# Performance work log

Measured on AMD Instinct MI355X. Metric: run time of the kernel, lower is better.

## Reference

```python
import jax, jax.numpy as jnp
import numpy as np
from jax import lax

NB = 8        # num_branch
K1 = 64       # == K2
NPOINT = 1024 # FPS samples
EPS = 1e-5    # BatchNorm eps


def setup_inputs() -> dict:
    key = jax.random.key(0)
    ks = jax.random.split(key, 40)
    B, L, F = 32, 512, 256
    Npart = 32768
    s = 0.05
    p = lambda k, sh: jax.random.normal(k, sh, jnp.float32) * s
    g = lambda k, sh: 1.0 + jax.random.normal(k, sh, jnp.float32) * 0.05
    inp = {}
    inp['x'] = jax.random.normal(ks[0], (B, L, F), jnp.float32)
    inp['x_part'] = jax.random.normal(ks[1], (B, Npart, 3), jnp.float32)
    # MappingNet params (stacked over NB branches)
    inp['mW1'] = p(ks[2], (NB, 512, 256)); inp['mb1'] = p(ks[3], (NB, 512))
    inp['mg1'] = g(ks[4], (NB, 512));      inp['mB1'] = p(ks[5], (NB, 512))
    inp['mW2'] = p(ks[6], (NB, 512, 512)); inp['mb2'] = p(ks[7], (NB, 512))
    inp['mg2'] = g(ks[8], (NB, 512));      inp['mB2'] = p(ks[9], (NB, 512))
    inp['mW3'] = p(ks[10], (NB, 512, 512)); inp['mb3'] = p(ks[11], (NB, 512))
    inp['mg3'] = g(ks[12], (NB, 512));      inp['mB3'] = p(ks[13], (NB, 512))
    inp['mW4'] = p(ks[14], (NB, K1, 512));  inp['mb4'] = p(ks[15], (NB, K1))
    inp['mg4'] = g(ks[16], (NB, K1));       inp['mB4'] = p(ks[17], (NB, K1))
    # AXform params (1x1 Conv1d == channel matmul), stacked over NB branches
    inp['aW1'] = p(ks[18], (NB, 64, K1));   inp['ab1'] = p(ks[19], (NB, 64))
    inp['ag1'] = g(ks[20], (NB, 64));       inp['aB1'] = p(ks[21], (NB, 64))
    inp['aW2'] = p(ks[22], (NB, 128, 64));  inp['ab2'] = p(ks[23], (NB, 128))
    inp['ag2'] = g(ks[24], (NB, 128));      inp['aB2'] = p(ks[25], (NB, 128))
    inp['aW3'] = p(ks[26], (NB, 128, 128)); inp['ab3'] = p(ks[27], (NB, 128))
    inp['aW4'] = p(ks[28], (NB, 3, K1));    inp['ab4'] = p(ks[29], (NB, 3))
    return inp


def _bn_feat(h, gam, bet):
    # BatchNorm1d (training-mode) over a [B, L, C] tensor, per channel C
    m = jnp.mean(h, axis=(0, 1))
    v = jnp.mean((h - m) ** 2, axis=(0, 1))
    return gam * (h - m) / jnp.sqrt(v + EPS) + bet


def _bn_ch(h, gam, bet):
    # BatchNorm1d (training-mode) over a [B, C, L] tensor, per channel C
    m = jnp.mean(h, axis=(0, 2), keepdims=True)
    v = jnp.mean((h - m) ** 2, axis=(0, 2), keepdims=True)
    return gam[None, :, None] * (h - m) / jnp.sqrt(v + EPS) + bet[None, :, None]


def _fps_indices(xyz, npoint):
    # Iterative farthest-point sampling: sequential min-distance updates
    B, N, _ = xyz.shape
    def step(carry, _):
        dist, far = carry
        c = jnp.take_along_axis(xyz, far[:, None, None], axis=1)  # [B,1,3]
        d = jnp.sum((xyz - c) ** 2, axis=-1)                      # [B,N]
        dist = jnp.minimum(dist, d)
        return (dist, jnp.argmax(dist, axis=-1).astype(jnp.int32)), far
    init = (jnp.full((B, N), 1e10, xyz.dtype), jnp.zeros((B,), jnp.int32))
    _, idx = lax.scan(step, init, None, length=npoint)  # [npoint, B]
    return idx.T  # [B, npoint]


def _branch(prm, x):
    (mW1, mb1, mg1, mB1, mW2, mb2, mg2, mB2, mW3, mb3, mg3, mB3,
     mW4, mb4, mg4, mB4, aW1, ab1, ag1, aB1, aW2, ab2, ag2, aB2,
     aW3, ab3, aW4, ab4) = prm
    # MappingNet: x [B,L,256] -> [B,L,K1]
    h = jax.nn.relu(_bn_feat(x @ mW1.T + mb1, mg1, mB1))
    h = jax.nn.relu(_bn_feat(h @ mW2.T + mb2, mg2, mB2))
    h = jax.nn.relu(_bn_feat(h @ mW3.T + mb3, mg3, mB3))
    h = jax.nn.relu(_bn_feat(h @ mW4.T + mb4, mg4, mB4))  # [B,L,K1]
    base = h
    # AXform
    t = jax.nn.relu(_bn_ch(jnp.einsum('oc,blc->bol', aW1, h) + ab1[:, None], ag1, aB1))
    t = jax.nn.relu(_bn_ch(jnp.einsum('oc,bcl->bol', aW2, t) + ab2[:, None], ag2, aB2))
    t = jnp.einsum('oc,bcl->bol', aW3, t) + ab3[:, None]   # [B,128,L]
    w = jax.nn.softmax(t, axis=2)
    pts = jnp.einsum('bml,blk->bmk', w, base)              # [B,128,K1]
    out = jnp.einsum('ok,bkm->bom', aW4, pts.transpose(0, 2, 1)) + ab4[:, None]  # [B,3,128]
    return out.transpose(0, 2, 1)  # [B,128,3]


def reference(x, x_part, mW1, mb1, mg1, mB1, mW2, mb2, mg2, mB2,
              mW3, mb3, mg3, mB3, mW4, mb4, mg4, mB4,
              aW1, ab1, ag1, aB1, aW2, ab2, ag2, aB2, aW3, ab3, aW4, ab4):
    B = x_part.shape[0]
    idx = _fps_indices(x_part, NPOINT)                     # [B,1024]
    x_partial = jnp.take_along_axis(x_part, idx[:, :, None], axis=1)  # [B,1024,3]
    prm = (mW1, mb1, mg1, mB1, mW2, mb2, mg2, mB2, mW3, mb3, mg3, mB3,
           mW4, mb4, mg4, mB4, aW1, ab1, ag1, aB1, aW2, ab2, ag2, aB2,
           aW3, ab3, aW4, ab4)
    outs = jax.vmap(_branch, in_axes=(0, None))(prm, x)    # [NB,B,128,3]
    x_1 = outs.transpose(1, 0, 2, 3).reshape(B, NB * 128, 3)
    return jnp.concatenate([x_1, x_partial], axis=1)       # [B,2048,3]
```

## Files before the change

### kernel.cpp

```cpp
#include <hip/hip_runtime.h>

typedef unsigned short u16;
typedef unsigned long long u64;
using bf16x8 = __attribute__((ext_vector_type(8))) short;
using f32x4  = __attribute__((ext_vector_type(4))) float;

#define NBR 8
#define BATCH 32
#define LSEQ 512
#define MROWS (BATCH*LSEQ)
#define NPART 32768

__device__ __forceinline__ u16 f2bf(float f) {
  unsigned u = __float_as_uint(f);
  unsigned r = u + 0x7fffu + ((u >> 16) & 1u);
  return (u16)(r >> 16);
}
__device__ __forceinline__ float bf2f(u16 s) {
  return __uint_as_float(((unsigned)s) << 16);
}

__global__ void cvt_kernel(const float* __restrict__ src, u16* __restrict__ dst, int n) {
  int i = blockIdx.x * blockDim.x + threadIdx.x;
  int stride = gridDim.x * blockDim.x;
  for (; i < n; i += stride) dst[i] = f2bf(src[i]);
}

__global__ __launch_bounds__(1024) void fps_kernel(const float* __restrict__ xp,
                                                   float* __restrict__ out,
                                                   u64* __restrict__ slots) {
  int w = blockIdx.x;
  int b = blockIdx.y;
  int tid = threadIdx.x;
  const float* P = xp + (size_t)b * NPART * 3;
  u64* slot = slots + (size_t)b * 8192;

  __shared__ u64 part[16];
  __shared__ float cb[3];

  float px[4], py[4], pz[4], dv[4];
#pragma unroll
  for (int k = 0; k < 4; k++) {
    int p = (w << 12) + (k << 10) + tid;
    px[k] = P[3*p]; py[k] = P[3*p+1]; pz[k] = P[3*p+2];
    dv[k] = 1e10f;
  }
  float cx = P[0], cy = P[1], cz = P[2];
  if (w == 0 && tid == 0) {
    float* o = out + ((size_t)b*2048 + 1024) * 3;
    o[0] = cx; o[1] = cy; o[2] = cz;
  }

  int lane = tid & 63, wv = tid >> 6;
  for (int it = 1; it < 1024; it++) {
    float best = -1.0f; int bk = 0;
#pragma unroll
    for (int k = 0; k < 4; k++) {
      float dx = __fsub_rn(px[k], cx);
      float dy = __fsub_rn(py[k], cy);
      float dz = __fsub_rn(pz[k], cz);
      float d = __fadd_rn(__fadd_rn(__fmul_rn(dx,dx), __fmul_rn(dy,dy)), __fmul_rn(dz,dz));
      float nd = fminf(dv[k], d);
      dv[k] = nd;
      if (nd > best) { best = nd; bk = k; }
    }
    unsigned pidx = (unsigned)((w << 12) + (bk << 10) + tid);
    u64 pk = ((u64)__float_as_uint(best) << 32) | (u64)(0xFFFFFFFFu - pidx);

#define DPP_STEP(CTRL) { \
    unsigned lo2 = (unsigned)__builtin_amdgcn_update_dpp(0, (int)(unsigned)(pk & 0xffffffffull), CTRL, 0xF, 0xF, true); \
    unsigned hi2 = (unsigned)__builtin_amdgcn_update_dpp(0, (int)(unsigned)(pk >> 32), CTRL, 0xF, 0xF, true); \
    u64 o = ((u64)hi2 << 32) | lo2; \
    if (o > pk) pk = o; }
    DPP_STEP(0x111) DPP_STEP(0x112) DPP_STEP(0x114) DPP_STEP(0x118)
    DPP_STEP(0x142) DPP_STEP(0x143)
#undef DPP_STEP
    unsigned rlo = (unsigned)__builtin_amdgcn_readlane((int)(unsigned)(pk & 0xffffffffull), 63);
    unsigned rhi = (unsigned)__builtin_amdgcn_readlane((int)(unsigned)(pk >> 32), 63);
    if (lane == 0) part[wv] = ((u64)rhi << 32) | rlo;
    __syncthreads();

    if (wv == 0) {
      u64 pv = part[lane & 15];
#pragma unroll
      for (int off = 1; off < 16; off <<= 1) {
        u64 o = __shfl_xor(pv, off);
        if (o > pv) pv = o;
      }
      if (lane == 0) {
        atomicExch(&slot[it*8 + w], pv);
      }
      u64 v;
      do {
        v = __hip_atomic_load(&slot[it*8 + (lane & 7)], __ATOMIC_RELAXED,
                              __HIP_MEMORY_SCOPE_AGENT);
      } while (!__all(v != 0));
#pragma unroll
      for (int off = 1; off < 8; off <<= 1) {
        u64 o = __shfl_xor(v, off);
        if (o > v) v = o;
      }
      if (lane == 0) {
        unsigned widx = 0xFFFFFFFFu - (unsigned)(v & 0xFFFFFFFFull);
        const float* pw = P + 3*(size_t)widx;
        float sx = pw[0], sy = pw[1], sz = pw[2];
        cb[0] = sx; cb[1] = sy; cb[2] = sz;
        if (w == 0) {
          float* o = out + ((size_t)b*2048 + 1024 + it) * 3;
          o[0] = sx; o[1] = sy; o[2] = sz;
        }
      }
    }
    __syncthreads();
    cx = cb[0]; cy = cb[1]; cz = cb[2];
  }
}

__global__ __launch_bounds__(256, 2) void gemm_bn(
    const u16* __restrict__ A, size_t strideA,
    const u16* __restrict__ W, size_t strideW,
    u16* __restrict__ Y, size_t strideY,
    float* __restrict__ statsOut,
    const float* __restrict__ statsIn,
    const float* __restrict__ gam, const float* __restrict__ bet,
    int N, int K, int bnA)
{
  int z = blockIdx.z;
  const u16* Ab = A + (size_t)z * strideA;
  const u16* Wb = W + (size_t)z * strideW;
  u16* Yb = Y + (size_t)z * strideY;
  int m0 = blockIdx.x * 128;
  int n0 = blockIdx.y * 128;

  __shared__ u16 As[128][72];
  __shared__ u16 Bs[128][72];
  __shared__ float sAl[512];
  __shared__ float sBe[512];

  int tid = threadIdx.x;
  if (bnA) {
    for (int ch = tid; ch < K; ch += 256) {
      float s  = statsIn[(size_t)z*1024 + ch*2];
      float sq = statsIn[(size_t)z*1024 + ch*2 + 1];
      float mean = s * (1.0f/16384.0f);
      float var  = sq * (1.0f/16384.0f) - mean*mean;
      float rs = rsqrtf(var + 1e-5f);
      float al = gam[(size_t)z*K + ch] * rs;
      sAl[ch] = al;
      sBe[ch] = bet[(size_t)z*K + ch] - al*mean;
    }
  }

  f32x4 acc[4][4] = {};
  int lane = tid & 63;
  int wave = tid >> 6;
  int wm = (wave & 1) * 64;
  int wn = (wave >> 1) * 64;
  int lm = lane & 15;
  int lq = lane >> 4;

  for (int k0 = 0; k0 < K; k0 += 64) {
    __syncthreads();
#pragma unroll
    for (int i = 0; i < 4; i++) {
      int f = i*256 + tid;
      int row = f >> 3;
      int kc = (f & 7) * 8;
      uint4 raw = *(const uint4*)(Ab + (size_t)(m0 + row) * K + (k0 + kc));
      if (bnA) {
        u16 us[8]; *(uint4*)us = raw;
        u16 ot[8];
#pragma unroll
        for (int e = 0; e < 8; e++) {
          float v = sAl[k0 + kc + e] * bf2f(us[e]) + sBe[k0 + kc + e];
          ot[e] = f2bf(fmaxf(v, 0.0f));
        }
        *(uint4*)(&As[row][kc]) = *(uint4*)ot;
      } else {
        *(uint4*)(&As[row][kc]) = raw;
      }
    }
#pragma unroll
    for (int i = 0; i < 4; i++) {
      int f = i*256 + tid;
      int row = f >> 3;
      int kc = (f & 7) * 8;
      uint4 v = {0u, 0u, 0u, 0u};
      if (n0 + row < N) v = *(const uint4*)(Wb + (size_t)(n0 + row) * K + (k0 + kc));
      *(uint4*)(&Bs[row][kc]) = v;
    }
    __syncthreads();
#pragma unroll
    for (int kk = 0; kk < 64; kk += 32) {
      bf16x8 af[4], bq[4];
#pragma unroll
      for (int t = 0; t < 4; t++) {
        af[t] = *(const bf16x8*)(&As[wm + t*16 + lm][kk + lq*8]);
        bq[t] = *(const bf16x8*)(&Bs[wn + t*16 + lm][kk + lq*8]);
      }
#pragma unroll
      for (int mt = 0; mt < 4; mt++) {
#pragma unroll
        for (int nt = 0; nt < 4; nt++) {
          acc[mt][nt] = __builtin_amdgcn_mfma_f32_16x16x32_bf16(af[mt], bq[nt], acc[mt][nt], 0, 0, 0);
        }
      }
    }
  }

#pragma unroll
  for (int mt = 0; mt < 4; mt++) {
#pragma unroll
    for (int nt = 0; nt < 4; nt++) {
      int colg = n0 + wn + nt*16 + lm;
      if (colg < N) {
#pragma unroll
        for (int r = 0; r < 4; r++) {
          int rowg = m0 + wm + mt*16 + lq*4 + r;
          Yb[(size_t)rowg * N + colg] = f2bf(acc[mt][nt][r]);
        }
      }
    }
  }
  if (statsOut) {
#pragma unroll
    for (int nt = 0; nt < 4; nt++) {
      float s = 0.f, sq = 0.f;
#pragma unroll
      for (int mt = 0; mt < 4; mt++) {
#pragma unroll
        for (int r = 0; r < 4; r++) { float v = acc[mt][nt][r]; s += v; sq += v*v; }
      }
      s  += __shfl_xor(s, 16);  s  += __shfl_xor(s, 32);
      sq += __shfl_xor(sq, 16); sq += __shfl_xor(sq, 32);
      int colg = n0 + wn + nt*16 + lm;
      if (lq == 0 && colg < N) {
        atomicAdd(&statsOut[(size_t)z*1024 + colg*2],     s);
        atomicAdd(&statsOut[(size_t)z*1024 + colg*2 + 1], sq);
      }
    }
  }
}

__global__ __launch_bounds__(256, 1) void finale_kernel(
    const u16* __restrict__ h4,
    const u16* __restrict__ t3,
    const float* __restrict__ stats4,
    const float* __restrict__ mg4, const float* __restrict__ mB4,
    const float* __restrict__ aW4, const float* __restrict__ ab4,
    float* __restrict__ out)
{
  int b = blockIdx.x, g = blockIdx.y;
  int tid = threadIdx.x;
  __shared__ u16 base_s[512*64];
  __shared__ u16 wbuf[512*64];
  __shared__ float ptsb[64*64];
  __shared__ float2 abl[64];
  __shared__ float red[4*64];
  __shared__ float colmax[64];
  __shared__ float colinv[64];

  if (tid < 64) {
    float s  = stats4[(size_t)g*1024 + tid*2];
    float sq = stats4[(size_t)g*1024 + tid*2 + 1];
    float mean = s * (1.0f/16384.0f);
    float var  = sq * (1.0f/16384.0f) - mean*mean;
    float rs = rsqrtf(var + 1e-5f);
    float al = mg4[g*64 + tid] * rs;
    abl[tid] = make_float2(al, mB4[g*64 + tid] - al*mean);
  }
  __syncthreads();

  const u16* h4b = h4 + ((size_t)g*MROWS + b*LSEQ) * 64;
  for (int i = 0; i < 16; i++) {
    int u = i*256 + tid;
    int l = u >> 3;
    int kc = (u & 7) * 8;
    uint4 raw = *(const uint4*)(h4b + (size_t)l*64 + kc);
    u16 us[8]; *(uint4*)us = raw;
    u16 ot[8];
#pragma unroll
    for (int e = 0; e < 8; e++) {
      float2 p = abl[kc + e];
      float v = p.x * bf2f(us[e]) + p.y;
      ot[e] = f2bf(fmaxf(v, 0.0f));
    }
    *(uint4*)(&base_s[l*64 + kc]) = *(uint4*)ot;
  }

  int col = tid & 63;
  int ts  = tid >> 6;
  int mch0 = (tid & 31) * 2;
  int k0 = (tid >> 5) * 8;

  for (int half = 0; half < 2; half++) {
    __syncthreads();
    const u16* t3b = t3 + ((size_t)g*MROWS + b*LSEQ) * 128 + half*64;
    for (int i = 0; i < 16; i++) {
      int u = i*256 + tid;
      int l = u >> 3;
      int kc = (u & 7) * 8;
      *(uint4*)(&wbuf[l*64 + kc]) = *(const uint4*)(t3b + (size_t)l*128 + kc);
    }
    __syncthreads();
    float mx = -1e30f;
    for (int j = 0; j < 128; j++) {
      int l = ts + j*4;
      mx = fmaxf(mx, bf2f(wbuf[l*64 + col]));
    }
    red[ts*64 + col] = mx;
    __syncthreads();
    if (ts == 0)
      colmax[col] = fmaxf(fmaxf(red[col], red[64+col]), fmaxf(red[128+col], red[192+col]));
    __syncthreads();
    mx = colmax[col];
    float sm = 0.0f;
    for (int j = 0; j < 128; j++) {
      int l = ts + j*4;
      float e = __expf(bf2f(wbuf[l*64 + col]) - mx);
      sm += e;
      wbuf[l*64 + col] = f2bf(e);
    }
    red[ts*64 + col] = sm;
    __syncthreads();
    if (ts == 0)
      colinv[col] = 1.0f / (red[col] + red[64+col] + red[128+col] + red[192+col]);
    __syncthreads();

    float a0[8] = {}, a1[8] = {};
    for (int l = 0; l < 512; l++) {
      unsigned wvv = *(const unsigned*)(&wbuf[l*64 + mch0]);
      float w0 = __uint_as_float((wvv & 0xffffu) << 16);
      float w1 = __uint_as_float((wvv >> 16) << 16);
      u16 bs[8]; *(uint4*)bs = *(const uint4*)(&base_s[l*64 + k0]);
#pragma unroll
      for (int e = 0; e < 8; e++) {
        float bv = bf2f(bs[e]);
        a0[e] = fmaf(w0, bv, a0[e]);
        a1[e] = fmaf(w1, bv, a1[e]);
      }
    }
    float i0 = colinv[mch0], i1 = colinv[mch0 + 1];
#pragma unroll
    for (int e = 0; e < 8; e++) {
      ptsb[mch0*64 + k0 + e]       = a0[e] * i0;
      ptsb[(mch0+1)*64 + k0 + e]   = a1[e] * i1;
    }
    __syncthreads();
    if (tid < 64) {
      const float* w4 = aW4 + (size_t)g*192;
      float o0 = ab4[g*3], o1 = ab4[g*3+1], o2 = ab4[g*3+2];
      for (int k = 0; k < 64; k++) {
        float pv = ptsb[tid*64 + k];
        o0 = fmaf(w4[k],      pv, o0);
        o1 = fmaf(w4[64 + k], pv, o1);
        o2 = fmaf(w4[128 + k],pv, o2);
      }
      float* op = out + ((size_t)b*2048 + g*128 + half*64 + tid) * 3;
      op[0] = o0; op[1] = o1; op[2] = o2;
    }
  }
}

extern "C" void kernel_launch(void* const* d_in, const int* in_sizes, int n_in,
                              void* d_out, int out_size, void* d_ws, size_t ws_size,
                              hipStream_t stream)
{
  (void)in_sizes; (void)n_in; (void)out_size; (void)ws_size;
  const float* x    = (const float*)d_in[0];
  const float* xprt = (const float*)d_in[1];
  const float* mW1 = (const float*)d_in[2];
  const float* mg1 = (const float*)d_in[4];
  const float* mB1 = (const float*)d_in[5];
  const float* mW2 = (const float*)d_in[6];
  const float* mg2 = (const float*)d_in[8];
  const float* mB2 = (const float*)d_in[9];
  const float* mW3 = (const float*)d_in[10];
  const float* mg3 = (const float*)d_in[12];
  const float* mB3 = (const float*)d_in[13];
  const float* mW4 = (const float*)d_in[14];
  const float* mg4 = (const float*)d_in[16];
  const float* mB4 = (const float*)d_in[17];
  const float* aW1 = (const float*)d_in[18];
  const float* ag1 = (const float*)d_in[20];
  const float* aB1 = (const float*)d_in[21];
  const float* aW2 = (const float*)d_in[22];
  const float* ag2 = (const float*)d_in[24];
  const float* aB2 = (const float*)d_in[25];
  const float* aW3 = (const float*)d_in[26];
  const float* aW4 = (const float*)d_in[28];
  const float* ab4 = (const float*)d_in[29];
  float* out = (float*)d_out;

  char* ws = (char*)d_ws;
  size_t off = 0;
  auto carve = [&](size_t bytes) -> char* {
    char* p = ws + off;
    off += (bytes + 255) & ~(size_t)255;
    return p;
  };
  u16* xb   = (u16*)carve((size_t)MROWS*256*2);
  u16* w1b  = (u16*)carve((size_t)NBR*512*256*2);
  u16* w2b  = (u16*)carve((size_t)NBR*512*512*2);
  u16* w3b  = (u16*)carve((size_t)NBR*512*512*2);
  u16* w4b  = (u16*)carve((size_t)NBR*64*512*2);
  u16* aw1b = (u16*)carve((size_t)NBR*64*64*2);
  u16* aw2b = (u16*)carve((size_t)NBR*128*64*2);
  u16* aw3b = (u16*)carve((size_t)NBR*128*128*2);
  u16* hA   = (u16*)carve((size_t)2*MROWS*512*2);
  u16* hB   = (u16*)carve((size_t)2*MROWS*512*2);
  u16* h4   = (u16*)carve((size_t)NBR*MROWS*64*2);
  u16* t1   = (u16*)carve((size_t)NBR*MROWS*64*2);
  float* stats = (float*)carve((size_t)6*NBR*1024*4);
  u64* slots = (u64*)carve((size_t)BATCH*8192*8);
  u16* t2 = hB;
  u16* t3 = hA;

  cvt_kernel<<<1024, 256, 0, stream>>>(x,   xb,   MROWS*256);
  cvt_kernel<<<1024, 256, 0, stream>>>(mW1, w1b,  NBR*512*256);
  cvt_kernel<<<1024, 256, 0, stream>>>(mW2, w2b,  NBR*512*512);
  cvt_kernel<<<1024, 256, 0, stream>>>(mW3, w3b,  NBR*512*512);
  cvt_kernel<<<1024, 256, 0, stream>>>(mW4, w4b,  NBR*64*512);
  cvt_kernel<<<256,  256, 0, stream>>>(aW1, aw1b, NBR*64*64);
  cvt_kernel<<<256,  256, 0, stream>>>(aW2, aw2b, NBR*128*64);
  cvt_kernel<<<256,  256, 0, stream>>>(aW3, aw3b, NBR*128*128);
  hipMemsetAsync(stats, 0, (size_t)6*NBR*1024*4, stream);
  hipMemsetAsync(slots, 0, (size_t)BATCH*8192*8, stream);

  fps_kernel<<<dim3(8, BATCH), 1024, 0, stream>>>(xprt, out, slots);

  for (int p = 0; p < 4; p++) {
    size_t g0 = (size_t)p * 2;
    gemm_bn<<<dim3(128,4,2), 256, 0, stream>>>(
      xb, (size_t)0, w1b + g0*512*256, (size_t)512*256,
      hA, (size_t)MROWS*512,
      stats + 0*NBR*1024 + g0*1024,
      (const float*)nullptr, (const float*)nullptr, (const float*)nullptr,
      512, 256, 0);
    gemm_bn<<<dim3(128,4,2), 256, 0, stream>>>(
      hA, (size_t)MROWS*512, w2b + g0*512*512, (size_t)512*512,
      hB, (size_t)MROWS*512,
      stats + 1*NBR*1024 + g0*1024,
      stats + 0*NBR*1024 + g0*1024, mg1 + g0*512, mB1 + g0*512,
      512, 512, 1);
    gemm_bn<<<dim3(128,4,2), 256, 0, stream>>>(
      hB, (size_t)MROWS*512, w3b + g0*512*512, (size_t)512*512,
      hA, (size_t)MROWS*512,
      stats + 2*NBR*1024 + g0*1024,
      stats + 1*NBR*1024 + g0*1024, mg2 + g0*512, mB2 + g0*512,
      512, 512, 1);
    gemm_bn<<<dim3(128,1,2), 256, 0, stream>>>(
      hA, (size_t)MROWS*512, w4b + g0*64*512, (size_t)64*512,
      h4 + g0*MROWS*64, (size_t)MROWS*64,
      stats + 3*NBR*1024 + g0*1024,
      stats + 2*NBR*1024 + g0*1024, mg3 + g0*512, mB3 + g0*512,
      64, 512, 1);
  }

  gemm_bn<<<dim3(128,1,8), 256, 0, stream>>>(
    h4, (size_t)MROWS*64, aw1b, (size_t)64*64,
    t1, (size_t)MROWS*64,
    stats + 4*NBR*1024,
    stats + 3*NBR*1024, mg4, mB4,
    64, 64, 1);
  gemm_bn<<<dim3(128,1,8), 256, 0, stream>>>(
    t1, (size_t)MROWS*64, aw2b, (size_t)128*64,
    t2, (size_t)MROWS*128,
    stats + 5*NBR*1024,
    stats + 4*NBR*1024, ag1, aB1,
    128, 64, 1);
  gemm_bn<<<dim3(128,1,8), 256, 0, stream>>>(
    t2, (size_t)MROWS*128, aw3b, (size_t)128*128,
    t3, (size_t)MROWS*128,
    (float*)nullptr,
    stats + 5*NBR*1024, ag2, aB2,
    128, 128, 1);

  finale_kernel<<<dim3(32,8), 256, 0, stream>>>(
    h4, t3, stats + 3*NBR*1024, mg4, mB4, aW4, ab4, out);
}
```

Before: 3.253 ms.

## Batch all branches per GEMM launch and split BN-ReLU into separate pass

When the workspace is large enough, each MLP layer now runs as a single GEMM launch over all 8 branches instead of four launches of two branches each. The BatchNorm+ReLU of the previous layer's output is moved out of the GEMM A-load into a standalone elementwise kernel that writes an activated bf16 copy. The GEMM launch bound is raised to allow 4 blocks per CU. The change adds full-size intermediate buffers and an extra read/write pass over every activation, in exchange for fewer launches, wider grids and a simpler GEMM inner loop.

After: 2.989 ms. 8.1% less time.

```diff
diff --git a/kernel.cpp b/kernel.cpp
--- a/kernel.cpp
+++ b/kernel.cpp
@@ -116,7 +116,44 @@
   }
 }
 
-__global__ __launch_bounds__(256, 2) void gemm_bn(
+__global__ __launch_bounds__(256) void bn_relu_kernel(
+    const u16* __restrict__ raw, u16* __restrict__ act,
+    const float* __restrict__ stats,
+    const float* __restrict__ gam, const float* __restrict__ bet,
+    int C, int chunksPerZ)
+{
+  int z = blockIdx.y;
+  __shared__ float sAl[512];
+  __shared__ float sBe[512];
+  for (int c = threadIdx.x; c < C; c += 256) {
+    float s  = stats[(size_t)z*1024 + c*2];
+    float sq = stats[(size_t)z*1024 + c*2 + 1];
+    float mean = s * (1.0f/16384.0f);
+    float var  = sq * (1.0f/16384.0f) - mean*mean;
+    float rs = rsqrtf(var + 1e-5f);
+    float al = gam[(size_t)z*C + c] * rs;
+    sAl[c] = al;
+    sBe[c] = bet[(size_t)z*C + c] - al*mean;
+  }
+  __syncthreads();
+  const u16* rz = raw + (size_t)z * chunksPerZ * 8;
+  u16* az = act + (size_t)z * chunksPerZ * 8;
+  int cm = C - 1;
+  for (int i = blockIdx.x*256 + threadIdx.x; i < chunksPerZ; i += gridDim.x*256) {
+    int c0 = (i * 8) & cm;
+    uint4 r = *(const uint4*)(rz + (size_t)i*8);
+    u16 us[8]; *(uint4*)us = r;
+    u16 ot[8];
+#pragma unroll
+    for (int e = 0; e < 8; e++) {
+      float v = sAl[c0+e] * bf2f(us[e]) + sBe[c0+e];
+      ot[e] = f2bf(fmaxf(v, 0.0f));
+    }
+    *(uint4*)(az + (size_t)i*8) = *(uint4*)ot;
+  }
+}
+
+__global__ __launch_bounds__(256, 4) void gemm_bn(
     const u16* __restrict__ A, size_t strideA,
     const u16* __restrict__ W, size_t strideW,
     u16* __restrict__ Y, size_t strideY,
@@ -366,7 +403,7 @@
                               void* d_out, int out_size, void* d_ws, size_t ws_size,
                               hipStream_t stream)
 {
-  (void)in_sizes; (void)n_in; (void)out_size; (void)ws_size;
+  (void)in_sizes; (void)n_in; (void)out_size;
   const float* x    = (const float*)d_in[0];
   const float* xprt = (const float*)d_in[1];
   const float* mW1 = (const float*)d_in[2];
@@ -407,14 +444,12 @@
   u16* aw1b = (u16*)carve((size_t)NBR*64*64*2);
   u16* aw2b = (u16*)carve((size_t)NBR*128*64*2);
   u16* aw3b = (u16*)carve((size_t)NBR*128*128*2);
-  u16* hA   = (u16*)carve((size_t)2*MROWS*512*2);
-  u16* hB   = (u16*)carve((size_t)2*MROWS*512*2);
-  u16* h4   = (u16*)carve((size_t)NBR*MROWS*64*2);
-  u16* t1   = (u16*)carve((size_t)NBR*MROWS*64*2);
   float* stats = (float*)carve((size_t)6*NBR*1024*4);
   u64* slots = (u64*)carve((size_t)BATCH*8192*8);
-  u16* t2 = hB;
-  u16* t3 = hA;
+  size_t commonOff = off;
+
+  size_t bigNeed = commonOff + 2*((size_t)NBR*MROWS*512*2 + 256) + 2*((size_t)NBR*MROWS*64*2 + 256);
+  bool bigPath = (ws_size >= bigNeed);
 
   cvt_kernel<<<1024, 256, 0, stream>>>(x,   xb,   MROWS*256);
   cvt_kernel<<<1024, 256, 0, stream>>>(mW1, w1b,  NBR*512*256);
@@ -429,53 +464,87 @@
 
   fps_kernel<<<dim3(8, BATCH), 1024, 0, stream>>>(xprt, out, slots);
 
-  for (int p = 0; p < 4; p++) {
-    size_t g0 = (size_t)p * 2;
-    gemm_bn<<<dim3(128,4,2), 256, 0, stream>>>(
-      xb, (size_t)0, w1b + g0*512*256, (size_t)512*256,
-      hA, (size_t)MROWS*512,
-      stats + 0*NBR*1024 + g0*1024,
-      (const float*)nullptr, (const float*)nullptr, (const float*)nullptr,
-      512, 256, 0);
-    gemm_bn<<<dim3(128,4,2), 256, 0, stream>>>(
-      hA, (size_t)MROWS*512, w2b + g0*512*512, (size_t)512*512,
-      hB, (size_t)MROWS*512,
-      stats + 1*NBR*1024 + g0*1024,
-      stats + 0*NBR*1024 + g0*1024, mg1 + g0*512, mB1 + g0*512,
-      512, 512, 1);
-    gemm_bn<<<dim3(128,4,2), 256, 0, stream>>>(
-      hB, (size_t)MROWS*512, w3b + g0*512*512, (size_t)512*512,
-      hA, (size_t)MROWS*512,
-      stats + 2*NBR*1024 + g0*1024,
-      stats + 1*NBR*1024 + g0*1024, mg2 + g0*512, mB2 + g0*512,
-      512, 512, 1);
-    gemm_bn<<<dim3(128,1,2), 256, 0, stream>>>(
-      hA, (size_t)MROWS*512, w4b + g0*64*512, (size_t)64*512,
-      h4 + g0*MROWS*64, (size_t)MROWS*64,
-      stats + 3*NBR*1024 + g0*1024,
-      stats + 2*NBR*1024 + g0*1024, mg3 + g0*512, mB3 + g0*512,
-      64, 512, 1);
-  }
-
-  gemm_bn<<<dim3(128,1,8), 256, 0, stream>>>(
-    h4, (size_t)MROWS*64, aw1b, (size_t)64*64,
-    t1, (size_t)MROWS*64,
-    stats + 4*NBR*1024,
-    stats + 3*NBR*1024, mg4, mB4,
-    64, 64, 1);
-  gemm_bn<<<dim3(128,1,8), 256, 0, stream>>>(
-    t1, (size_t)MROWS*64, aw2b, (size_t)128*64,
-    t2, (size_t)MROWS*128,
-    stats + 5*NBR*1024,
-    stats + 4*NBR*1024, ag1, aB1,
-    128, 64, 1);
-  gemm_bn<<<dim3(128,1,8), 256, 0, stream>>>(
-    t2, (size_t)MROWS*128, aw3b, (size_t)128*128,
-    t3, (size_t)MROWS*128,
-    (float*)nullptr,
-    stats + 5*NBR*1024, ag2, aB2,
-    128, 128, 1);
-
-  finale_kernel<<<dim3(32,8), 256, 0, stream>>>(
-    h4, t3, stats + 3*NBR*1024, mg4, mB4, aW4, ab4, out);
-}
+  if (bigPath) {
+    u16* hR  = (u16*)carve((size_t)NBR*MROWS*512*2);
+    u16* hA  = (u16*)carve((size_t)NBR*MROWS*512*2);
+    u16* h4  = (u16*)carve((size_t)NBR*MROWS*64*2);
+    u16* h4a = (u16*)carve((size_t)NBR*MROWS*64*2);
+    u16* t1r = hR;
+    u16* t1a = hA;
+    u16* t2r = hR + (size_t)NBR*MROWS*128;
+    u16* t2a = hA + (size_t)NBR*MROWS*128;
+    u16* t3  = hA + (size_t)2*NBR*MROWS*128;
+
+    const int bigChunks = MROWS*512/8, smChunks = MROWS*64/8, mdChunks = MROWS*128/8;
+
+    gemm_bn<<<dim3(128,4,8), 256, 0, stream>>>(
+      xb, (size_t)0, w1b, (size_t)512*256, hR, (size_t)MROWS*512,
+      stats + 0*NBR*1024, nullptr, nullptr, nullptr, 512, 256, 0);
+    bn_relu_kernel<<<dim3(1024,8), 256, 0, stream>>>(hR, hA, stats + 0*NBR*1024, mg1, mB1, 512, bigChunks);
+    gemm_bn<<<dim3(128,4,8), 256, 0, stream>>>(
+      hA, (size_t)MROWS*512, w2b, (size_t)512*512, hR, (size_t)MROWS*512,
+      stats + 1*NBR*1024, nullptr, nullptr, nullptr, 512, 512, 0);
+    bn_relu_kernel<<<dim3(1024,8), 256, 0, stream>>>(hR, hA, stats + 1*NBR*1024, mg2, mB2, 512, bigChunks);
+    gemm_bn<<<dim3(128,4,8), 256, 0, stream>>>(
+      hA, (size_t)MROWS*512, w3b, (size_t)512*512, hR, (size_t)MROWS*512,
+      stats + 2*NBR*1024, nullptr, nullptr, nullptr, 512, 512, 0);
+    bn_relu_kernel<<<dim3(1024,8), 256, 0, stream>>>(hR, hA, stats + 2*NBR*1024, mg3, mB3, 512, bigChunks);
+    gemm_bn<<<dim3(128,1,8), 256, 0, stream>>>(
+      hA, (size_t)MROWS*512, w4b, (size_t)64*512, h4, (size_t)MROWS*64,
+      stats + 3*NBR*1024, nullptr, nullptr, nullptr, 64, 512, 0);
+    bn_relu_kernel<<<dim3(256,8), 256, 0, stream>>>(h4, h4a, stats + 3*NBR*1024, mg4, mB4, 64, smChunks);
+    gemm_bn<<<dim3(128,1,8), 256, 0, stream>>>(
+      h4a, (size_t)MROWS*64, aw1b, (size_t)64*64, t1r, (size_t)MROWS*64,
+      stats + 4*NBR*1024, nullptr, nullptr, nullptr, 64, 64, 0);
+    bn_relu_kernel<<<dim3(256,8), 256, 0, stream>>>(t1r, t1a, stats + 4*NBR*1024, ag1, aB1, 64, smChunks);
+    gemm_bn<<<dim3(128,1,8), 256, 0, stream>>>(
+      t1a, (size_t)MROWS*64, aw2b, (size_t)128*64, t2r, (size_t)MROWS*128,
+      stats + 5*NBR*1024, nullptr, nullptr, nullptr, 128, 64, 0);
+    bn_relu_kernel<<<dim3(512,8), 256, 0, stream>>>(t2r, t2a, stats + 5*NBR*1024, ag2, aB2, 128, mdChunks);
+    gemm_bn<<<dim3(128,1,8), 256, 0, stream>>>(
+      t2a, (size_t)MROWS*128, aw3b, (size_t)128*128, t3, (size_t)MROWS*128,
+      nullptr, nullptr, nullptr, nullptr, 128, 128, 0);
+
+    finale_kernel<<<dim3(32,8), 256, 0, stream>>>(
+      h4, t3, stats + 3*NBR*1024, mg4, mB4, aW4, ab4, out);
+  } else {
+    u16* hA = (u16*)carve((size_t)2*MROWS*512*2);
+    u16* hB = (u16*)carve((size_t)2*MROWS*512*2);
+    u16* h4 = (u16*)carve((size_t)NBR*MROWS*64*2);
+    u16* t1 = (u16*)carve((size_t)NBR*MROWS*64*2);
+    u16* t2 = hB;
+    u16* t3 = hA;
+
+    for (int p = 0; p < 4; p++) {
+      size_t g0 = (size_t)p * 2;
+      gemm_bn<<<dim3(128,4,2), 256, 0, stream>>>(
+        xb, (size_t)0, w1b + g0*512*256, (size_t)512*256, hA, (size_t)MROWS*512,
+        stats + 0*NBR*1024 + g0*1024, nullptr, nullptr, nullptr, 512, 256, 0);
+      gemm_bn<<<dim3(128,4,2), 256, 0, stream>>>(
+        hA, (size_t)MROWS*512, w2b + g0*512*512, (size_t)512*512, hB, (size_t)MROWS*512,
+        stats + 1*NBR*1024 + g0*1024,
+        stats + 0*NBR*1024 + g0*1024, mg1 + g0*512, mB1 + g0*512, 512, 512, 1);
+      gemm_bn<<<dim3(128,4,2), 256, 0, stream>>>(
+        hB, (size_t)MROWS*512, w3b + g0*512*512, (size_t)512*512, hA, (size_t)MROWS*512,
+        stats + 2*NBR*1024 + g0*1024,
+        stats + 1*NBR*1024 + g0*1024, mg2 + g0*512, mB2 + g0*512, 512, 512, 1);
+      gemm_bn<<<dim3(128,1,2), 256, 0, stream>>>(
+        hA, (size_t)MROWS*512, w4b + g0*64*512, (size_t)64*512,
+        h4 + g0*MROWS*64, (size_t)MROWS*64,
+        stats + 3*NBR*1024 + g0*1024,
+        stats + 2*NBR*1024 + g0*1024, mg3 + g0*512, mB3 + g0*512, 64, 512, 1);
+    }
+    gemm_bn<<<dim3(128,1,8), 256, 0, stream>>>(
+      h4, (size_t)MROWS*64, aw1b, (size_t)64*64, t1, (size_t)MROWS*64,
+      stats + 4*NBR*1024, stats + 3*NBR*1024, mg4, mB4, 64, 64, 1);
+    gemm_bn<<<dim3(128,1,8), 256, 0, stream>>>(
+      t1, (size_t)MROWS*64, aw2b, (size_t)128*64, t2, (size_t)MROWS*128,
+      stats + 5*NBR*1024, stats + 4*NBR*1024, ag1, aB1, 128, 64, 1);
+    gemm_bn<<<dim3(128,1,8), 256, 0, stream>>>(
+      t2, (size_t)MROWS*128, aw3b, (size_t)128*128, t3, (size_t)MROWS*128,
+      nullptr, stats + 5*NBR*1024, ag2, aB2, 128, 128, 1);
+
+    finale_kernel<<<dim3(32,8), 256, 0, stream>>>(
+      h4, t3, stats + 3*NBR*1024, mg4, mB4, aW4, ab4, out);
+  }
+}
```
